# Optimization experiments

Measured on AMD Instinct MI355X. Metric: run time of the kernel, lower is better.

Reference implementation:

```python
import jax, jax.numpy as jnp
import numpy as np

D_IN, H, NH = 256, 512, 8
B, T = 8, 1024


def sinusoidal_pe(seq_len, d_model):
    pos = jnp.arange(seq_len, dtype=jnp.float32)[:, None]
    div = jnp.exp(jnp.arange(0, d_model, 2, dtype=jnp.float32) * (-jnp.log(10000.0) / d_model))
    pe = jnp.zeros((seq_len, d_model), jnp.float32)
    pe = pe.at[:, 0::2].set(jnp.sin(pos * div)).at[:, 1::2].set(jnp.cos(pos * div))
    return pe


def layer_norm(x, g, b, eps=1e-5):
    mu = jnp.mean(x, -1, keepdims=True)
    var = jnp.mean((x - mu) ** 2, -1, keepdims=True)
    return (x - mu) * jax.lax.rsqrt(var + eps) * g + b


def lstm_dir(x, wih, whh, bih, bhh):
    # x: [B,T,H]; wih/whh: [4H,H]; gate order i,f,g,o (PyTorch convention)
    Bx = x.shape[0]
    Hh = whh.shape[1]
    xg = jnp.einsum('bth,gh->btg', x, wih) + bih  # precompute input gates [B,T,4H]

    def step(carry, xg_t):
        h, c = carry
        gates = xg_t + h @ whh.T + bhh
        i, f, g, o = jnp.split(gates, 4, axis=-1)
        c = jax.nn.sigmoid(f) * c + jax.nn.sigmoid(i) * jnp.tanh(g)
        h = jax.nn.sigmoid(o) * jnp.tanh(c)
        return (h, c), h

    h0 = jnp.zeros((Bx, Hh), x.dtype)
    _, hs = jax.lax.scan(step, (h0, h0), xg.transpose(1, 0, 2))
    return hs.transpose(1, 0, 2)  # [B,T,H]


def setup_inputs():
    key = jax.random.key(0)
    ks = jax.random.split(key, 30)
    s = 0.02

    def g(k, shape):
        return jax.random.normal(k, shape, jnp.float32) * s

    return {
        'temporal_data': jax.random.normal(ks[0], (B, T, D_IN), jnp.float32),
        'w_in': g(ks[1], (H, D_IN)), 'b_in': jnp.zeros((H,), jnp.float32),
        'wq': g(ks[2], (H, H)), 'bq': jnp.zeros((H,), jnp.float32),
        'wk': g(ks[3], (H, H)), 'bk': jnp.zeros((H,), jnp.float32),
        'wv': g(ks[4], (H, H)), 'bv': jnp.zeros((H,), jnp.float32),
        'wo': g(ks[5], (H, H)), 'bo': jnp.zeros((H,), jnp.float32),
        'g1': jnp.ones((H,), jnp.float32), 'b1': jnp.zeros((H,), jnp.float32),
        'wih_f': g(ks[6], (4 * H, H)), 'whh_f': g(ks[7], (4 * H, H)),
        'bih_f': jnp.zeros((4 * H,), jnp.float32), 'bhh_f': jnp.zeros((4 * H,), jnp.float32),
        'wih_b': g(ks[8], (4 * H, H)), 'whh_b': g(ks[9], (4 * H, H)),
        'bih_b': jnp.zeros((4 * H,), jnp.float32), 'bhh_b': jnp.zeros((4 * H,), jnp.float32),
        'g2': jnp.ones((2 * H,), jnp.float32), 'b2': jnp.zeros((2 * H,), jnp.float32),
        'w_out': g(ks[10], (H, 2 * H)), 'b_out': jnp.zeros((H,), jnp.float32),
    }


def reference(temporal_data, w_in, b_in, wq, bq, wk, bk, wv, bv, wo, bo, g1, b1,
              wih_f, whh_f, bih_f, bhh_f, wih_b, whh_b, bih_b, bhh_b, g2, b2, w_out, b_out):
    x = temporal_data @ w_in.T + b_in                      # [B,T,H]
    Bx, Tx, _ = x.shape
    x = x + sinusoidal_pe(Tx, H)
    residual = x

    hd = H // NH
    q = (x @ wq.T + bq).reshape(Bx, Tx, NH, hd).transpose(0, 2, 1, 3)
    k = (x @ wk.T + bk).reshape(Bx, Tx, NH, hd).transpose(0, 2, 1, 3)
    v = (x @ wv.T + bv).reshape(Bx, Tx, NH, hd).transpose(0, 2, 1, 3)
    scores = jnp.einsum('bhqd,bhkd->bhqk', q, k) * (hd ** -0.5)
    causal = jnp.triu(jnp.ones((Tx, Tx), bool), 1)
    scores = jnp.where(causal, jnp.float32(-1e9), scores)
    attn = jax.nn.softmax(scores, axis=-1)
    o = jnp.einsum('bhqk,bhkd->bhqd', attn, v).transpose(0, 2, 1, 3).reshape(Bx, Tx, H)
    o = o @ wo.T + bo

    x = layer_norm(o + residual, g1, b1)                   # dropout in eval = identity

    h_fwd = lstm_dir(x, wih_f, whh_f, bih_f, bhh_f)
    h_bwd = jnp.flip(lstm_dir(jnp.flip(x, 1), wih_b, whh_b, bih_b, bhh_b), 1)
    lstm_out = jnp.concatenate([h_fwd, h_bwd], axis=-1)    # [B,T,2H]
    lstm_out = layer_norm(lstm_out, g2, b2)

    emb = jnp.mean(lstm_out, axis=1)                       # [B,2H]
    return emb @ w_out.T + b_out                           # [B,H]
```

## Files before the change

### kernel.cpp

```cpp
#include <hip/hip_runtime.h>

typedef unsigned short u16;
typedef unsigned int   u32;
typedef unsigned long long u64;
typedef __attribute__((ext_vector_type(8))) short short8v;
typedef __attribute__((ext_vector_type(4))) float f32x4;

#define DINL __device__ __forceinline__

DINL u16 f2bf(float f){ union{float f;u32 u;} v{f}; return (u16)((v.u + 0x7fffu + ((v.u>>16)&1u))>>16); }
DINL float bf2f(u16 b){ union{u32 u;float f;} v{(u32)b<<16}; return v.f; }
DINL f32x4 MFMA16(short8v a, short8v b, f32x4 c){ return __builtin_amdgcn_mfma_f32_16x16x32_bf16(a,b,c,0,0,0); }
DINL void gl16(const void* g, void* l){
  __builtin_amdgcn_global_load_lds((const __attribute__((address_space(1))) void*)g,
                                   (__attribute__((address_space(3))) void*)l, 16, 0, 0);
}
DINL float wredd(float v){
#pragma unroll
  for (int m=1;m<64;m<<=1) v += __shfl_xor(v, m);
  return v;
}
DINL float sigm(float x){ return 1.f/(1.f+__expf(-x)); }
DINL float tanh_(float x){ return 2.f/(1.f+__expf(-2.f*x)) - 1.f; }

__global__ __launch_bounds__(256) void cvtk(const float* __restrict__ src, u16* __restrict__ dst, int n){
  int i = (blockIdx.x*256 + threadIdx.x)*4;
  float4 v = *(const float4*)(src + i);
  dst[i+0]=f2bf(v.x); dst[i+1]=f2bf(v.y); dst[i+2]=f2bf(v.z); dst[i+3]=f2bf(v.w);
}

template<int EPI>
__global__ __launch_bounds__(256) void gemm128(
    const u16* __restrict__ A, const u16* __restrict__ W,
    const float* __restrict__ bias0, const float* __restrict__ bias1, const float* __restrict__ bias2,
    const u16* __restrict__ resid, u16* __restrict__ out, int M, int N, int K)
{
  __shared__ __align__(16) u16 Al[128*64];
  __shared__ __align__(16) u16 Bl[128*64];
  const int tid = threadIdx.x, lane = tid & 63, w = tid >> 6;
  const int wr = w >> 1, wc = w & 1;
  const int m0 = blockIdx.y * 128, n0 = blockIdx.x * 128;
  f32x4 acc[4][4] = {};
  for (int k0 = 0; k0 < K; k0 += 64) {
#pragma unroll
    for (int j = 0; j < 4; ++j) {
      int idx = (j*4 + w)*64 + lane;
      int r = idx >> 3, c8 = idx & 7;
      gl16(A + (size_t)(m0 + r)*K + k0 + c8*8, (void*)(Al + (size_t)(j*4+w)*512));
      gl16(W + (size_t)(n0 + r)*K + k0 + c8*8, (void*)(Bl + (size_t)(j*4+w)*512));
    }
    __syncthreads();
#pragma unroll
    for (int kk = 0; kk < 2; ++kk) {
      short8v af[4], bf[4];
#pragma unroll
      for (int i = 0; i < 4; ++i)
        af[i] = *(const short8v*)(Al + ((wr*64 + i*16 + (lane&15))*64 + kk*32 + (lane>>4)*8));
#pragma unroll
      for (int i = 0; i < 4; ++i)
        bf[i] = *(const short8v*)(Bl + ((wc*64 + i*16 + (lane&15))*64 + kk*32 + (lane>>4)*8));
#pragma unroll
      for (int mi=0;mi<4;++mi)
#pragma unroll
        for (int ni=0;ni<4;++ni)
          acc[mi][ni] = MFMA16(af[mi], bf[ni], acc[mi][ni]);
    }
    __syncthreads();
  }
#pragma unroll
  for (int mi=0;mi<4;++mi)
#pragma unroll
    for (int ni=0;ni<4;++ni)
#pragma unroll
      for (int r=0;r<4;++r) {
        int m = m0 + wr*64 + mi*16 + (lane>>4)*4 + r;
        int n = n0 + wc*64 + ni*16 + (lane&15);
        float v = acc[mi][ni][r];
        if constexpr (EPI == 0) {
          int t = m & 1023;
          float ang = (float)t * expf((float)(n & ~1) * (-9.210340371976184f/512.f));
          v += bias0[n] + ((n & 1) ? cosf(ang) : sinf(ang));
          out[(size_t)m*512 + n] = f2bf(v);
        } else if constexpr (EPI == 1) {
          int g = n >> 9, n5 = n & 511, hh = n5 >> 6, dh = n5 & 63;
          v += (g==0 ? bias0 : g==1 ? bias1 : bias2)[n5];
          size_t bh = (size_t)((m>>10)*8 + hh);
          u16 val = f2bf(v);
          if (g == 0)      out[(bh*1024 + (m&1023))*64 + dh] = val;
          else if (g == 1) out[4194304 + (bh*1024 + (m&1023))*64 + dh] = val;
          else             out[8388608 + (bh*64 + dh)*1024 + (m&1023)] = val;
        } else {
          v += bias0[n] + bf2f(resid[(size_t)m*512 + n]);
          out[(size_t)m*512 + n] = f2bf(v);
        }
      }
}

__global__ __launch_bounds__(256) void attnk(const u16* __restrict__ qb, const u16* __restrict__ kb,
                                             const u16* __restrict__ vt, u16* __restrict__ attno)
{
  __shared__ __align__(16) u16 P[4][16][72];
  const int tid = threadIdx.x, lane = tid & 63, w = tid >> 6;
  const int bh = blockIdx.x >> 4, qblk = blockIdx.x & 15;
  const int b = bh >> 3, h = bh & 7;
  const float scale = 0.125f;
  short8v qf[2];
  {
    const u16* qbase = qb + ((size_t)bh*1024 + qblk*64 + w*16)*64;
#pragma unroll
    for (int kk=0;kk<2;++kk)
      qf[kk] = *(const short8v*)(qbase + (size_t)(lane&15)*64 + kk*32 + (lane>>4)*8);
  }
  f32x4 o[4] = {};
  float mrun[4], lrun[4];
#pragma unroll
  for (int r=0;r<4;++r){ mrun[r] = -1e30f; lrun[r] = 0.f; }
  for (int kblk = 0; kblk <= qblk; ++kblk) {
    f32x4 s[4] = {};
#pragma unroll
    for (int kk=0;kk<2;++kk)
#pragma unroll
      for (int nt=0;nt<4;++nt) {
        short8v kf = *(const short8v*)(kb + ((size_t)bh*1024 + kblk*64 + nt*16 + (lane&15))*64 + kk*32 + (lane>>4)*8);
        s[nt] = MFMA16(qf[kk], kf, s[nt]);
      }
    float pnew[4][4];
#pragma unroll
    for (int r=0;r<4;++r) {
      int q = qblk*64 + w*16 + (lane>>4)*4 + r;
      float sv[4]; float rowmax = -1e30f;
#pragma unroll
      for (int nt=0;nt<4;++nt) {
        int key = kblk*64 + nt*16 + (lane&15);
        float x = s[nt][r]*scale;
        if (key > q) x = -1e30f;
        sv[nt] = x; rowmax = fmaxf(rowmax, x);
      }
#pragma unroll
      for (int msk=1; msk<16; msk<<=1) rowmax = fmaxf(rowmax, __shfl_xor(rowmax, msk));
      float mnew = fmaxf(mrun[r], rowmax);
      float sf = __expf(mrun[r]-mnew);
      float psum = 0.f;
#pragma unroll
      for (int nt=0;nt<4;++nt){ float p = __expf(sv[nt]-mnew); pnew[nt][r]=p; psum += p; }
#pragma unroll
      for (int msk=1; msk<16; msk<<=1) psum += __shfl_xor(psum, msk);
      lrun[r] = lrun[r]*sf + psum;
      mrun[r] = mnew;
#pragma unroll
      for (int nt=0;nt<4;++nt) o[nt][r] *= sf;
    }
#pragma unroll
    for (int nt=0;nt<4;++nt)
#pragma unroll
      for (int r=0;r<4;++r)
        P[w][(lane>>4)*4+r][nt*16+(lane&15)] = f2bf(pnew[nt][r]);
#pragma unroll
    for (int kk=0;kk<2;++kk) {
      short8v pf = *(const short8v*)&P[w][lane&15][kk*32 + (lane>>4)*8];
#pragma unroll
      for (int nt=0;nt<4;++nt) {
        short8v vf = *(const short8v*)(vt + ((size_t)bh*64 + nt*16 + (lane&15))*1024 + kblk*64 + kk*32 + (lane>>4)*8);
        o[nt] = MFMA16(pf, vf, o[nt]);
      }
    }
  }
#pragma unroll
  for (int nt=0;nt<4;++nt)
#pragma unroll
    for (int r=0;r<4;++r) {
      int q = qblk*64 + w*16 + (lane>>4)*4 + r;
      int dh = nt*16 + (lane&15);
      attno[((size_t)b*1024 + q)*512 + h*64 + dh] = f2bf(o[nt][r] / lrun[r]);
    }
}

__global__ __launch_bounds__(256) void ln1k(const u16* __restrict__ pre, const float* __restrict__ g1,
                                            const float* __restrict__ b1, u16* __restrict__ xl){
  int row = blockIdx.x*4 + (threadIdx.x>>6), lane = threadIdx.x&63;
  short8v xv = *(const short8v*)(pre + (size_t)row*512 + lane*8);
  float v[8], s=0.f, s2=0.f;
#pragma unroll
  for (int e=0;e<8;++e){ v[e]=bf2f((u16)xv[e]); s+=v[e]; s2+=v[e]*v[e]; }
  s = wredd(s); s2 = wredd(s2);
  float mu = s*(1.f/512.f);
  float rs = rsqrtf(s2*(1.f/512.f) - mu*mu + 1e-5f);
  int b = row>>10, t = row&1023;
  short8v ov;
#pragma unroll
  for (int e=0;e<8;++e){ int c=lane*8+e; ov[e]=(short)f2bf((v[e]-mu)*rs*g1[c]+b1[c]); }
  *(short8v*)(xl + ((size_t)t*8 + b)*512 + lane*8) = ov;
}

__global__ __launch_bounds__(256) void lstmk(
    const u16* __restrict__ xl,
    const float* __restrict__ wih_f, const float* __restrict__ whh_f,
    const float* __restrict__ bih_f, const float* __restrict__ bhh_f,
    const float* __restrict__ wih_b, const float* __restrict__ whh_b,
    const float* __restrict__ bih_b, const float* __restrict__ bhh_b,
    u16* __restrict__ hc, u32* __restrict__ flg)
{
  extern __shared__ char smem[];
  u16*  WI  = (u16*)smem;
  u16*  WH  = (u16*)(smem + 65536);
  float* RED = (float*)(smem + 131072);
  u16*  HST = (u16*)(smem + 139264);

  const int tid = threadIdx.x, lane = tid&63, w = tid>>6;
  const int d = blockIdx.x >> 5, slice = blockIdx.x & 31, u0 = slice*16;
  const float* WIHg = d ? wih_b : wih_f;
  const float* WHHg = d ? whh_b : whh_f;
  const float* BIH  = d ? bih_b : bih_f;
  const float* BHH  = d ? bhh_b : bhh_f;

  for (int f = tid; f < 4096; f += 256) {
    int nt = f>>10, kc = (f>>6)&15, l = f&63;
    size_t grow = (size_t)(nt*512 + u0 + (l&15));
    int k = kc*32 + (l>>4)*8;
    const float* pi = WIHg + grow*512 + k;
    const float* ph = WHHg + grow*512 + k;
    short8v wa, wb;
#pragma unroll
    for (int e=0;e<8;++e){ wa[e]=(short)f2bf(pi[e]); wb[e]=(short)f2bf(ph[e]); }
    *(short8v*)(WI + (size_t)f*8) = wa;
    *(short8v*)(WH + (size_t)f*8) = wb;
  }
  __syncthreads();

  const bool act = tid < 128;
  const int b_ = tid>>4, u_ = tid&15;
  float c_state = 0.f, bias_c[4];
  if (act)
#pragma unroll
    for (int g=0;g<4;++g) bias_c[g] = BIH[g*512+u0+u_] + BHH[g*512+u0+u_];

  for (int t = 0; t < 1024; ++t) {
    int te = d ? 1023 - t : t;
    f32x4 acc[4] = {};
    {
      const u16* xb = xl + ((size_t)te*8 + (lane&7))*512;
#pragma unroll
      for (int kk=0;kk<4;++kk) {
        int kc = w*4 + kk;
        short8v xf = *(const short8v*)(xb + kc*32 + (lane>>4)*8);
#pragma unroll
        for (int nt=0;nt<4;++nt)
          acc[nt] = MFMA16(xf, *(const short8v*)(WI + ((size_t)(nt*16+kc)*64 + lane)*8), acc[nt]);
      }
    }
    if (t > 0) {
      if (w == 0) {
        const u32* fb = flg + ((size_t)d*1024 + (t-1))*32;
        u64 pend;
        do {
          u32 ok = (lane < 32) ? __hip_atomic_load(fb + lane, __ATOMIC_ACQUIRE, __HIP_MEMORY_SCOPE_AGENT) : 1u;
          pend = __ballot(ok == 0u);
          if (pend) __builtin_amdgcn_s_sleep(1);
        } while (pend);
      }
      __syncthreads();
      int tp = d ? 1024 - t : t - 1;
      const u16* hb = hc + ((size_t)d*1024 + tp)*4096 + (size_t)(lane&7)*512;
#pragma unroll
      for (int kk=0;kk<4;++kk) {
        int kc = w*4 + kk;
        short8v hf = *(const short8v*)(hb + kc*32 + (lane>>4)*8);
#pragma unroll
        for (int nt=0;nt<4;++nt)
          acc[nt] = MFMA16(hf, *(const short8v*)(WH + ((size_t)(nt*16+kc)*64 + lane)*8), acc[nt]);
      }
    }
    if (lane < 32)
#pragma unroll
      for (int nt=0;nt<4;++nt)
        *(f32x4*)(RED + ((size_t)(w*4+nt)*32 + lane)*4) = acc[nt];
    __syncthreads();
    if (act) {
      int lc = u_ + 16*(b_>>2), rg = b_&3;
      float gates[4];
#pragma unroll
      for (int g=0;g<4;++g) {
        float s = 0.f;
#pragma unroll
        for (int wv=0;wv<4;++wv) s += RED[((size_t)(wv*4+g)*32 + lc)*4 + rg];
        gates[g] = s + bias_c[g];
      }
      float ig = sigm(gates[0]), fg = sigm(gates[1]), gg = tanh_(gates[2]), og = sigm(gates[3]);
      c_state = fg*c_state + ig*gg;
      HST[b_*16 + u_] = f2bf(og * tanh_(c_state));
    }
    __syncthreads();
    if (tid < 32) {
      int b2 = tid>>2, q = tid&3;
      u64 v = *(const u64*)(HST + b2*16 + q*4);
      u64* dst = (u64*)(hc + ((size_t)d*1024 + te)*4096 + (size_t)b2*512 + u0 + q*4);
      __hip_atomic_store(dst, v, __ATOMIC_RELAXED, __HIP_MEMORY_SCOPE_AGENT);
    }
    __syncthreads();
    if (tid == 0)
      __hip_atomic_store(flg + ((size_t)d*1024 + t)*32 + slice, 1u, __ATOMIC_RELEASE, __HIP_MEMORY_SCOPE_AGENT);
  }
}

__global__ __launch_bounds__(256) void ln2k(const u16* __restrict__ hc, const float* __restrict__ g2,
                                            const float* __restrict__ b2, float* __restrict__ emb){
  __shared__ float accl[4][1024];
  int b = blockIdx.x>>4, chunk = blockIdx.x&15;
  int lane = threadIdx.x&63, w = threadIdx.x>>6;
  for (int i=lane;i<1024;i+=64) accl[w][i]=0.f;
#pragma unroll 1
  for (int i=0;i<16;++i) {
    int t = chunk*64 + w*16 + i;
    short8v xf = *(const short8v*)(hc + ((size_t)t*8 + b)*512 + lane*8);
    short8v xb = *(const short8v*)(hc + ((size_t)(1024+t)*8 + b)*512 + lane*8);
    float vf[8], vb[8], s=0.f, s2=0.f;
#pragma unroll
    for (int e=0;e<8;++e){ vf[e]=bf2f((u16)xf[e]); vb[e]=bf2f((u16)xb[e]);
                           s += vf[e]+vb[e]; s2 += vf[e]*vf[e]+vb[e]*vb[e]; }
    s = wredd(s); s2 = wredd(s2);
    float mu = s*(1.f/1024.f);
    float rs = rsqrtf(s2*(1.f/1024.f) - mu*mu + 1e-5f);
#pragma unroll
    for (int e=0;e<8;++e){
      int c = lane*8+e;
      accl[w][c]     += (vf[e]-mu)*rs*g2[c]     + b2[c];
      accl[w][512+c] += (vb[e]-mu)*rs*g2[512+c] + b2[512+c];
    }
  }
  __syncthreads();
  for (int c = threadIdx.x; c < 1024; c += 256)
    atomicAdd(emb + (size_t)b*1024 + c, accl[0][c]+accl[1][c]+accl[2][c]+accl[3][c]);
}

__global__ __launch_bounds__(256) void fink(const float* __restrict__ emb, const float* __restrict__ w_out,
                                            const float* __restrict__ b_out, float* __restrict__ out){
  int gid = blockIdx.x*256 + threadIdx.x;
  int n = gid>>3, b = gid&7;
  const float* e = emb + (size_t)b*1024;
  const float* wr = w_out + (size_t)n*1024;
  float s = 0.f;
  for (int k=0;k<1024;k+=4) {
    float4 ev = *(const float4*)(e+k);
    float4 wv = *(const float4*)(wr+k);
    s += ev.x*wv.x + ev.y*wv.y + ev.z*wv.z + ev.w*wv.w;
  }
  out[(size_t)b*512 + n] = b_out[n] + s*(1.f/1024.f);
}

#define OFF_FLG   0u
#define OFF_EMB   262144u
#define OFF_A0    327680u
#define OFF_WIN   4521984u
#define OFF_WQKV  4784128u
#define OFF_WO    6356992u
#define OFF_X0B   6881280u
#define OFF_QB    15269888u
#define OFF_ATT   40435712u
#define OFF_PRE   48824320u
#define OFF_XL    57212928u
#define OFF_HC    65601536u

extern "C" void kernel_launch(void* const* d_in, const int* in_sizes, int n_in,
                              void* d_out, int out_size, void* d_ws, size_t ws_size,
                              hipStream_t stream) {
  const float* temporal = (const float*)d_in[0];
  const float* w_in = (const float*)d_in[1];  const float* b_in = (const float*)d_in[2];
  const float* wq = (const float*)d_in[3];    const float* bq = (const float*)d_in[4];
  const float* wk = (const float*)d_in[5];    const float* bk = (const float*)d_in[6];
  const float* wv = (const float*)d_in[7];    const float* bv = (const float*)d_in[8];
  const float* wo = (const float*)d_in[9];    const float* bo = (const float*)d_in[10];
  const float* g1 = (const float*)d_in[11];   const float* b1 = (const float*)d_in[12];
  const float* wih_f = (const float*)d_in[13]; const float* whh_f = (const float*)d_in[14];
  const float* bih_f = (const float*)d_in[15]; const float* bhh_f = (const float*)d_in[16];
  const float* wih_b = (const float*)d_in[17]; const float* whh_b = (const float*)d_in[18];
  const float* bih_b = (const float*)d_in[19]; const float* bhh_b = (const float*)d_in[20];
  const float* g2 = (const float*)d_in[21];   const float* b2 = (const float*)d_in[22];
  const float* w_out = (const float*)d_in[23]; const float* b_out = (const float*)d_in[24];

  char* ws = (char*)d_ws;
  u32* FLG = (u32*)(ws + OFF_FLG);
  float* EMB = (float*)(ws + OFF_EMB);
  u16* A0   = (u16*)(ws + OFF_A0);
  u16* WIN  = (u16*)(ws + OFF_WIN);
  u16* WQKV = (u16*)(ws + OFF_WQKV);
  u16* WOb  = (u16*)(ws + OFF_WO);
  u16* X0B  = (u16*)(ws + OFF_X0B);
  u16* QB   = (u16*)(ws + OFF_QB);
  u16* ATT  = (u16*)(ws + OFF_ATT);
  u16* PRE  = (u16*)(ws + OFF_PRE);
  u16* XL   = (u16*)(ws + OFF_XL);
  u16* HC   = (u16*)(ws + OFF_HC);

  (void)hipFuncSetAttribute((const void*)lstmk, hipFuncAttributeMaxDynamicSharedMemorySize, 139520);

  hipMemsetAsync(ws, 0, 294912, stream);

  cvtk<<<2048,256,0,stream>>>(temporal, A0, 2097152);
  cvtk<<<128, 256,0,stream>>>(w_in, WIN, 131072);
  cvtk<<<256, 256,0,stream>>>(wq, WQKV,           262144);
  cvtk<<<256, 256,0,stream>>>(wk, WQKV + 262144,  262144);
  cvtk<<<256, 256,0,stream>>>(wv, WQKV + 524288,  262144);
  cvtk<<<256, 256,0,stream>>>(wo, WOb, 262144);

  gemm128<0><<<dim3(4,64), 256, 0, stream>>>(A0, WIN, b_in, nullptr, nullptr, nullptr, X0B, 8192, 512, 256);
  gemm128<1><<<dim3(12,64),256, 0, stream>>>(X0B, WQKV, bq, bk, bv, nullptr, QB, 8192, 1536, 512);
  attnk<<<1024,256,0,stream>>>(QB, QB + 4194304, QB + 8388608, ATT);
  gemm128<3><<<dim3(4,64), 256, 0, stream>>>(ATT, WOb, bo, nullptr, nullptr, X0B, PRE, 8192, 512, 512);
  ln1k<<<2048,256,0,stream>>>(PRE, g1, b1, XL);
  lstmk<<<64,256,139520,stream>>>(XL, wih_f, whh_f, bih_f, bhh_f, wih_b, whh_b, bih_b, bhh_b, HC, FLG);
  ln2k<<<128,256,0,stream>>>(HC, g2, b2, EMB);
  fink<<<16,256,0,stream>>>(EMB, w_out, b_out, (float*)d_out);
}
```

Measured before the change: 4.118 ms.

## Replace LSTM per-step flag barrier with tagged hidden-state words and double-buffered reduction

Each hidden value is now stored as a 32-bit word that packs the bf16 value with a timestep tag, so consumers poll the data itself instead of waiting on a separate per-slice flag array. This removes two block barriers, the LDS staging of h, and the release/acquire flag round trip from every recurrent step. The reduction buffer is double-buffered by step parity so one __syncthreads per step suffices. In exchange the hidden-state buffer doubles in size, a 32 MB memset is added each call, and consumers spin on many relaxed loads instead of one flag per slice.

```diff
diff --git a/kernel.cpp b/kernel.cpp
--- a/kernel.cpp
+++ b/kernel.cpp
@@ -198,13 +198,12 @@
     const float* __restrict__ bih_f, const float* __restrict__ bhh_f,
     const float* __restrict__ wih_b, const float* __restrict__ whh_b,
     const float* __restrict__ bih_b, const float* __restrict__ bhh_b,
-    u16* __restrict__ hc, u32* __restrict__ flg)
+    u32* __restrict__ ht)
 {
   extern __shared__ char smem[];
   u16*  WI  = (u16*)smem;
   u16*  WH  = (u16*)(smem + 65536);
   float* RED = (float*)(smem + 131072);
-  u16*  HST = (u16*)(smem + 139264);
 
   const int tid = threadIdx.x, lane = tid&63, w = tid>>6;
   const int d = blockIdx.x >> 5, slice = blockIdx.x & 31, u0 = slice*16;
@@ -235,13 +234,13 @@
     for (int g=0;g<4;++g) bias_c[g] = BIH[g*512+u0+u_] + BHH[g*512+u0+u_];
 
   for (int t = 0; t < 1024; ++t) {
-    int te = d ? 1023 - t : t;
+    const int te = d ? 1023 - t : t;
     f32x4 acc[4] = {};
     {
       const u16* xb = xl + ((size_t)te*8 + (lane&7))*512;
 #pragma unroll
       for (int kk=0;kk<4;++kk) {
-        int kc = w*4 + kk;
+        const int kc = w*4 + kk;
         short8v xf = *(const short8v*)(xb + kc*32 + (lane>>4)*8);
 #pragma unroll
         for (int nt=0;nt<4;++nt)
@@ -249,60 +248,69 @@
       }
     }
     if (t > 0) {
-      if (w == 0) {
-        const u32* fb = flg + ((size_t)d*1024 + (t-1))*32;
-        u64 pend;
-        do {
-          u32 ok = (lane < 32) ? __hip_atomic_load(fb + lane, __ATOMIC_ACQUIRE, __HIP_MEMORY_SCOPE_AGENT) : 1u;
-          pend = __ballot(ok == 0u);
-          if (pend) __builtin_amdgcn_s_sleep(1);
-        } while (pend);
-      }
-      __syncthreads();
-      int tp = d ? 1024 - t : t - 1;
-      const u16* hb = hc + ((size_t)d*1024 + tp)*4096 + (size_t)(lane&7)*512;
+      const int tp = d ? 1024 - t : t - 1;
+      const u32 tg = (u32)t;
+      const u32* hb = ht + ((size_t)(d*1024 + tp)*8 + (lane&7))*512 + (lane>>4)*8;
+      u64 hv[4][4];
+      u32 mask = 0;
+      for (;;) {
+#pragma unroll
+        for (int kk=0;kk<4;++kk) {
+          const u64* p = (const u64*)(hb + (w*4+kk)*32);
+#pragma unroll
+          for (int j=0;j<4;++j) {
+            const int bit = kk*4 + j;
+            if (!((mask >> bit) & 1u)) {
+              u64 v = __hip_atomic_load(p + j, __ATOMIC_RELAXED, __HIP_MEMORY_SCOPE_AGENT);
+              if ((u32)(v & 0xffffu) == tg && ((u32)(v >> 32) & 0xffffu) == tg) {
+                hv[kk][j] = v; mask |= (1u << bit);
+              }
+            }
+          }
+        }
+        if (__all(mask == 0xffffu)) break;
+        __builtin_amdgcn_s_sleep(1);
+      }
 #pragma unroll
       for (int kk=0;kk<4;++kk) {
-        int kc = w*4 + kk;
-        short8v hf = *(const short8v*)(hb + kc*32 + (lane>>4)*8);
+        short8v hf;
+#pragma unroll
+        for (int j=0;j<4;++j) {
+          hf[2*j]   = (short)((u32)hv[kk][j] >> 16);
+          hf[2*j+1] = (short)(hv[kk][j] >> 48);
+        }
+        const int kc = w*4 + kk;
 #pragma unroll
         for (int nt=0;nt<4;++nt)
           acc[nt] = MFMA16(hf, *(const short8v*)(WH + ((size_t)(nt*16+kc)*64 + lane)*8), acc[nt]);
       }
     }
+    float* R = RED + (size_t)(t & 1)*2048;
     if (lane < 32)
 #pragma unroll
       for (int nt=0;nt<4;++nt)
-        *(f32x4*)(RED + ((size_t)(w*4+nt)*32 + lane)*4) = acc[nt];
+        *(f32x4*)(R + ((size_t)(w*4+nt)*32 + lane)*4) = acc[nt];
     __syncthreads();
     if (act) {
-      int lc = u_ + 16*(b_>>2), rg = b_&3;
+      const int lc = u_ + 16*(b_>>2), rg = b_&3;
       float gates[4];
 #pragma unroll
       for (int g=0;g<4;++g) {
         float s = 0.f;
 #pragma unroll
-        for (int wv=0;wv<4;++wv) s += RED[((size_t)(wv*4+g)*32 + lc)*4 + rg];
+        for (int wv=0;wv<4;++wv) s += R[((size_t)(wv*4+g)*32 + lc)*4 + rg];
         gates[g] = s + bias_c[g];
       }
       float ig = sigm(gates[0]), fg = sigm(gates[1]), gg = tanh_(gates[2]), og = sigm(gates[3]);
       c_state = fg*c_state + ig*gg;
-      HST[b_*16 + u_] = f2bf(og * tanh_(c_state));
-    }
-    __syncthreads();
-    if (tid < 32) {
-      int b2 = tid>>2, q = tid&3;
-      u64 v = *(const u64*)(HST + b2*16 + q*4);
-      u64* dst = (u64*)(hc + ((size_t)d*1024 + te)*4096 + (size_t)b2*512 + u0 + q*4);
-      __hip_atomic_store(dst, v, __ATOMIC_RELAXED, __HIP_MEMORY_SCOPE_AGENT);
-    }
-    __syncthreads();
-    if (tid == 0)
-      __hip_atomic_store(flg + ((size_t)d*1024 + t)*32 + slice, 1u, __ATOMIC_RELEASE, __HIP_MEMORY_SCOPE_AGENT);
-  }
-}
-
-__global__ __launch_bounds__(256) void ln2k(const u16* __restrict__ hc, const float* __restrict__ g2,
+      u32 word = ((u32)f2bf(og * tanh_(c_state)) << 16) | (u32)(t + 1);
+      __hip_atomic_store(ht + ((size_t)(d*1024 + te)*8 + b_)*512 + u0 + u_, word,
+                         __ATOMIC_RELAXED, __HIP_MEMORY_SCOPE_AGENT);
+    }
+  }
+}
+
+__global__ __launch_bounds__(256) void ln2k(const u32* __restrict__ ht, const float* __restrict__ g2,
                                             const float* __restrict__ b2, float* __restrict__ emb){
   __shared__ float accl[4][1024];
   int b = blockIdx.x>>4, chunk = blockIdx.x&15;
@@ -311,12 +319,14 @@
 #pragma unroll 1
   for (int i=0;i<16;++i) {
     int t = chunk*64 + w*16 + i;
-    short8v xf = *(const short8v*)(hc + ((size_t)t*8 + b)*512 + lane*8);
-    short8v xb = *(const short8v*)(hc + ((size_t)(1024+t)*8 + b)*512 + lane*8);
+    const u32* pf = ht + ((size_t)t*8 + b)*512 + lane*8;
+    const u32* pb = ht + ((size_t)(1024+t)*8 + b)*512 + lane*8;
     float vf[8], vb[8], s=0.f, s2=0.f;
 #pragma unroll
-    for (int e=0;e<8;++e){ vf[e]=bf2f((u16)xf[e]); vb[e]=bf2f((u16)xb[e]);
-                           s += vf[e]+vb[e]; s2 += vf[e]*vf[e]+vb[e]*vb[e]; }
+    for (int e=0;e<8;++e){
+      vf[e]=bf2f((u16)(pf[e]>>16)); vb[e]=bf2f((u16)(pb[e]>>16));
+      s += vf[e]+vb[e]; s2 += vf[e]*vf[e]+vb[e]*vb[e];
+    }
     s = wredd(s); s2 = wredd(s2);
     float mu = s*(1.f/1024.f);
     float rs = rsqrtf(s2*(1.f/1024.f) - mu*mu + 1e-5f);
@@ -347,18 +357,17 @@
   out[(size_t)b*512 + n] = b_out[n] + s*(1.f/1024.f);
 }
 
-#define OFF_FLG   0u
-#define OFF_EMB   262144u
-#define OFF_A0    327680u
-#define OFF_WIN   4521984u
-#define OFF_WQKV  4784128u
-#define OFF_WO    6356992u
-#define OFF_X0B   6881280u
-#define OFF_QB    15269888u
-#define OFF_ATT   40435712u
-#define OFF_PRE   48824320u
-#define OFF_XL    57212928u
-#define OFF_HC    65601536u
+#define OFF_EMB   0u
+#define OFF_A0    32768u
+#define OFF_WIN   4227072u
+#define OFF_WQKV  4489216u
+#define OFF_WO    6062080u
+#define OFF_X0B   6586368u
+#define OFF_QB    14974976u
+#define OFF_PRE   14974976u
+#define OFF_XL    23363584u
+#define OFF_ATT   40140800u
+#define OFF_HT    48529408u
 
 extern "C" void kernel_launch(void* const* d_in, const int* in_sizes, int n_in,
                               void* d_out, int out_size, void* d_ws, size_t ws_size,
@@ -378,7 +387,6 @@
   const float* w_out = (const float*)d_in[23]; const float* b_out = (const float*)d_in[24];
 
   char* ws = (char*)d_ws;
-  u32* FLG = (u32*)(ws + OFF_FLG);
   float* EMB = (float*)(ws + OFF_EMB);
   u16* A0   = (u16*)(ws + OFF_A0);
   u16* WIN  = (u16*)(ws + OFF_WIN);
@@ -386,14 +394,15 @@
   u16* WOb  = (u16*)(ws + OFF_WO);
   u16* X0B  = (u16*)(ws + OFF_X0B);
   u16* QB   = (u16*)(ws + OFF_QB);
-  u16* ATT  = (u16*)(ws + OFF_ATT);
   u16* PRE  = (u16*)(ws + OFF_PRE);
   u16* XL   = (u16*)(ws + OFF_XL);
-  u16* HC   = (u16*)(ws + OFF_HC);
-
-  (void)hipFuncSetAttribute((const void*)lstmk, hipFuncAttributeMaxDynamicSharedMemorySize, 139520);
-
-  hipMemsetAsync(ws, 0, 294912, stream);
+  u16* ATT  = (u16*)(ws + OFF_ATT);
+  u32* HT   = (u32*)(ws + OFF_HT);
+
+  (void)hipFuncSetAttribute((const void*)lstmk, hipFuncAttributeMaxDynamicSharedMemorySize, 147456);
+
+  hipMemsetAsync(ws + OFF_EMB, 0, 32768, stream);
+  hipMemsetAsync(ws + OFF_HT, 0, 33554432, stream);
 
   cvtk<<<2048,256,0,stream>>>(temporal, A0, 2097152);
   cvtk<<<128, 256,0,stream>>>(w_in, WIN, 131072);
@@ -407,7 +416,7 @@
   attnk<<<1024,256,0,stream>>>(QB, QB + 4194304, QB + 8388608, ATT);
   gemm128<3><<<dim3(4,64), 256, 0, stream>>>(ATT, WOb, bo, nullptr, nullptr, X0B, PRE, 8192, 512, 512);
   ln1k<<<2048,256,0,stream>>>(PRE, g1, b1, XL);
-  lstmk<<<64,256,139520,stream>>>(XL, wih_f, whh_f, bih_f, bhh_f, wih_b, whh_b, bih_b, bhh_b, HC, FLG);
-  ln2k<<<128,256,0,stream>>>(HC, g2, b2, EMB);
+  lstmk<<<64,256,147456,stream>>>(XL, wih_f, whh_f, bih_f, bhh_f, wih_b, whh_b, bih_b, bhh_b, HT);
+  ln2k<<<128,256,0,stream>>>(HT, g2, b2, EMB);
   fink<<<16,256,0,stream>>>(EMB, w_out, b_out, (float*)d_out);
 }
```

After: 5.400 ms. 1.31x slower.
